# Optimization experiments

Hardware: AMD Instinct MI355X
Metric: run time of the kernel (lower is better)

The kernel has to match this reference:

```python
import jax, jax.numpy as jnp
import numpy as np

R, B, D, H, N, F = 8, 16, 32, 128, 2048, 256
HALF_LOG_2PI = np.float32(0.9189385332046727)  # 0.5*log(2*pi)


def _made_masks():
    # MADE masks for a 2-hidden-layer network (D -> H -> H -> 2*D), params=2,
    # input_order='random' per (region, batch) network, hidden degrees cyclic in [1, D-1].
    rng = np.random.RandomState(0)
    deg_in = np.stack([np.stack([rng.permutation(D) + 1 for _ in range(B)]) for _ in range(R)])  # [R,B,D]
    h_deg = (np.arange(H) % (D - 1)) + 1  # [H]
    M1 = (deg_in[:, :, :, None] <= h_deg[None, None, None, :]).astype(np.float32)  # [R,B,D,H]
    M2 = np.broadcast_to((h_deg[:, None] <= h_deg[None, :]).astype(np.float32), (R, B, H, H)).copy()  # [R,B,H,H]
    out_deg = np.repeat(deg_in, 2, axis=-1)  # [R,B,2D]; index k=2*d+p matches reshape(...,D,2)
    M3 = (h_deg[None, None, :, None] < out_deg[:, :, None, :]).astype(np.float32)  # [R,B,H,2D]
    return M1, M2, M3


def setup_inputs() -> dict:
    key = jax.random.key(0)
    k1, k2, k3, k4 = jax.random.split(key, 4)
    x = jax.random.normal(k1, (N, F), dtype=jnp.float32)
    W1 = jax.random.normal(k2, (R, B, D, H), dtype=jnp.float32) * 0.1
    W2 = jax.random.normal(k3, (R, B, H, H), dtype=jnp.float32) * 0.05
    W3 = jax.random.normal(k4, (R, B, H, 2 * D), dtype=jnp.float32) * 0.02
    M1, M2, M3 = _made_masks()
    region_idx = jnp.arange(F, dtype=jnp.int64 if jax.config.jax_enable_x64 else jnp.int32).reshape(R, D)
    return {"x": x, "W1": W1, "W2": W2, "W3": W3,
            "M1": jnp.asarray(M1), "M2": jnp.asarray(M2), "M3": jnp.asarray(M3),
            "region_idx": region_idx}


def reference(x, W1, W2, W3, M1, M2, M3, region_idx):
    # Gather per-region features: [N, R, D] -> [R, N, D]
    xr = jnp.transpose(x[:, region_idx], (1, 0, 2))
    # Masked MADE forward (no bias, relu), batched over all R*B networks.
    h1 = jax.nn.relu(jnp.einsum('rnd,rbdh->rbnh', xr, W1 * M1))
    h2 = jax.nn.relu(jnp.einsum('rbnh,rbhk->rbnk', h1, W2 * M2))
    out = jnp.einsum('rbnk,rbko->rbno', h2, W3 * M3)  # [R,B,N,2D]
    out = out.reshape(out.shape[0], out.shape[1], out.shape[2], -1, 2)  # [R,B,N,D,2]
    shift, log_scale = out[..., 0], out[..., 1]
    # MAF inverse (one pass): u = (y - shift) * exp(-log_scale);
    # log_prob = sum_d Normal(0,1).log_prob(u_d) - log_scale_d
    u = (xr[:, None] - shift) * jnp.exp(-log_scale)  # [R,B,N,D]
    ll = jnp.sum(-0.5 * u * u - HALF_LOG_2PI - log_scale, axis=-1)  # [R,B,N]
    return jnp.transpose(ll, (2, 0, 1))  # [N, R, B]
```

## Files before the change

### kernel.cpp

```cpp
#include <hip/hip_runtime.h>
#include <math.h>

constexpr int R_ = 8;
constexpr int B_ = 16;
constexpr int D_ = 32;
constexpr int H_ = 128;
constexpr int N_ = 2048;
constexpr int F_ = 256;
constexpr int O_ = 64;
constexpr float HLP_ = 0.9189385332046727f;

typedef float f32x4 __attribute__((ext_vector_type(4)));
typedef short bf16x8 __attribute__((ext_vector_type(8)));
typedef unsigned uint32x4 __attribute__((ext_vector_type(4)));

__device__ __forceinline__ unsigned pk2(float lo, float hi) {
    unsigned a = __builtin_bit_cast(unsigned, lo) + 0x8000u;
    unsigned b = __builtin_bit_cast(unsigned, hi) + 0x8000u;
    return __builtin_amdgcn_perm(b, a, 0x07060302);
}

__global__ __launch_bounds__(256, 1)
void flow_all(const float* __restrict__ x,
              const float* __restrict__ W1, const float* __restrict__ W2,
              const float* __restrict__ W3,
              const float* __restrict__ M1, const float* __restrict__ M2,
              const float* __restrict__ M3,
              const int* __restrict__ ridx,
              float* __restrict__ out)
{
    __shared__ __align__(16) unsigned short stg[2][5120];
    __shared__ __align__(16) unsigned short hws[4][8192];

    const int bid = blockIdx.x;
    const int rb  = bid >> 1;
    const int hf  = bid & 1;
    const int r   = rb >> 4;

    const int t    = threadIdx.x;
    const int lane = t & 63;
    const int w    = t >> 6;
    const int q    = lane >> 4;
    const int c    = lane & 15;

    unsigned short* hwp = hws[w];

    const int nbase = hf * 1024 + w * 256 + c;
    const int xoff = r * 32 + q * 8;

    auto xload = [&](int row, float* g) {
        const float* p0 = x + (size_t)row * F_ + xoff;
        float4 f0 = *(const float4*)p0;
        float4 f1 = *(const float4*)(p0 + 4);
        g[0] = f0.x; g[1] = f0.y; g[2] = f0.z; g[3] = f0.w;
        g[4] = f1.x; g[5] = f1.y; g[6] = f1.z; g[7] = f1.w;
    };

    float g0A[8], g0B[8], g1A[8], g1B[8];
    xload(nbase, g0A);
    xload(nbase + 16, g0B);

    bf16x8 a1[8], a2[4][8], a3[4][4];
    {
        const float* W1b = W1 + (size_t)rb * 32 * 128;
        const float* M1b = M1 + (size_t)rb * 32 * 128;
        const float* W2b = W2 + (size_t)rb * 128 * 128;
        const float* M2s = M2;
        const float* W3b = W3 + (size_t)rb * 128 * 64;
        const float* M3b = M3 + (size_t)rb * 128 * 64;

        const int pm  = t & 127, pkh = t >> 7;
        const int qm  = t & 63,  qk  = t >> 6;
        int osrc;
        {
            int dp = qm >> 1, pb = qm & 1;
            int dsrc = ((dp >> 1) & 3) * 8 + (dp >> 3) * 2 + (dp & 1);
            osrc = dsrc * 2 + pb;
        }

        float wv[2][16], mv[2][16];
        auto slab_load = [&](int s, float* wvv, float* mvv) {
            if (s == 0) {
                const float* wp = W1b + (size_t)(pkh * 16) * 128 + pm;
                const float* mp = M1b + (size_t)(pkh * 16) * 128 + pm;
#pragma unroll
                for (int e = 0; e < 16; ++e) { wvv[e] = wp[(size_t)e * 128]; mvv[e] = mp[(size_t)e * 128]; }
            } else if (s <= 4) {
                const float* wp = W2b + (size_t)((s - 1) * 32 + pkh * 16) * 128 + pm;
                const float* mp = M2s + (size_t)((s - 1) * 32 + pkh * 16) * 128 + pm;
#pragma unroll
                for (int e = 0; e < 16; ++e) { wvv[e] = wp[(size_t)e * 128]; mvv[e] = mp[(size_t)e * 128]; }
            } else {
                int ss = s - 5;
                const float* wp = W3b + (size_t)(ss * 64 + qk * 16) * 64 + osrc;
                const float* mp = M3b + (size_t)(ss * 64 + qk * 16) * 64 + osrc;
#pragma unroll
                for (int e = 0; e < 16; ++e) { wvv[e] = wp[(size_t)e * 64]; mvv[e] = mp[(size_t)e * 64]; }
            }
        };
        auto slab_store = [&](int s, const float* wvv, const float* mvv) {
            unsigned u[8];
#pragma unroll
            for (int e2 = 0; e2 < 8; ++e2)
                u[e2] = pk2(wvv[2 * e2] * mvv[2 * e2], wvv[2 * e2 + 1] * mvv[2 * e2 + 1]);
            uint32x4 ulo = {u[0], u[1], u[2], u[3]};
            uint32x4 uhi = {u[4], u[5], u[6], u[7]};
            unsigned short* st = stg[s & 1];
            if (s <= 4) {
                *(uint32x4*)&st[pm * 40 + pkh * 16]     = ulo;
                *(uint32x4*)&st[pm * 40 + pkh * 16 + 8] = uhi;
            } else {
                *(uint32x4*)&st[qm * 72 + qk * 16]     = ulo;
                *(uint32x4*)&st[qm * 72 + qk * 16 + 8] = uhi;
            }
        };

        slab_load(0, wv[0], mv[0]);
#pragma unroll
        for (int s = 0; s < 7; ++s) {
            if (s < 6) slab_load(s + 1, wv[(s + 1) & 1], mv[(s + 1) & 1]);
            slab_store(s, wv[s & 1], mv[s & 1]);
            __syncthreads();
            const unsigned short* st = stg[s & 1];
            if (s == 0) {
#pragma unroll
                for (int mt = 0; mt < 8; ++mt)
                    a1[mt] = *(const bf16x8*)&st[(mt * 16 + c) * 40 + q * 8];
            } else if (s <= 4) {
#pragma unroll
                for (int mt = 0; mt < 8; ++mt)
                    a2[s - 1][mt] = *(const bf16x8*)&st[(mt * 16 + c) * 40 + q * 8];
            } else {
                int ss = s - 5;
#pragma unroll
                for (int mt3 = 0; mt3 < 4; ++mt3) {
                    a3[ss * 2 + 0][mt3] = *(const bf16x8*)&st[(mt3 * 16 + c) * 72 + 0  + q * 8];
                    a3[ss * 2 + 1][mt3] = *(const bf16x8*)&st[(mt3 * 16 + c) * 72 + 32 + q * 8];
                }
            }
        }
    }

    auto hstore = [&](int tau, int mt, const f32x4& v) {
        int ktw = mt >> 1;
        int qw  = (mt & 1) * 2 + (q >> 1);
        int j0  = (q & 1) * 4;
        unsigned lo = pk2(fmaxf(v[0], 0.f), fmaxf(v[1], 0.f));
        unsigned hi = pk2(fmaxf(v[2], 0.f), fmaxf(v[3], 0.f));
        *(uint2*)&hwp[(((tau * 4 + ktw) * 64) + qw * 16 + c) * 8 + j0] = make_uint2(lo, hi);
    };

    const f32x4 z = {0.f, 0.f, 0.f, 0.f};

    auto pass_body = [&](int p, int tb, const float* xA, const float* xB,
                         float* nA, float* nB) {
        uint32x4 uA = {pk2(xA[0], xA[1]), pk2(xA[2], xA[3]), pk2(xA[4], xA[5]), pk2(xA[6], xA[7])};
        uint32x4 uB = {pk2(xB[0], xB[1]), pk2(xB[2], xB[3]), pk2(xB[4], xB[5]), pk2(xB[6], xB[7])};
        bf16x8 xbA = __builtin_bit_cast(bf16x8, uA);
        bf16x8 xbB = __builtin_bit_cast(bf16x8, uB);

        {
            f32x4 accA[8], accB[8];
#pragma unroll
            for (int mt = 0; mt < 8; ++mt) {
                accA[mt] = __builtin_amdgcn_mfma_f32_16x16x32_bf16(a1[mt], xbA, z, 0, 0, 0);
                accB[mt] = __builtin_amdgcn_mfma_f32_16x16x32_bf16(a1[mt], xbB, z, 0, 0, 0);
            }
#pragma unroll
            for (int mt = 0; mt < 8; ++mt) { hstore(tb + 0, mt, accA[mt]); hstore(tb + 1, mt, accB[mt]); }
        }

        if (p < 7) {
            xload(nbase + (p + 1) * 32, nA);
            xload(nbase + (p + 1) * 32 + 16, nB);
        }

        {
            f32x4 c2A[8], c2B[8];
#pragma unroll
            for (int mt = 0; mt < 8; ++mt) { c2A[mt] = z; c2B[mt] = z; }
#pragma unroll
            for (int kt = 0; kt < 4; ++kt) {
                bf16x8 bA = *(const bf16x8*)&hwp[(((tb + 0) * 4 + kt) * 64 + lane) * 8];
                bf16x8 bB = *(const bf16x8*)&hwp[(((tb + 1) * 4 + kt) * 64 + lane) * 8];
#pragma unroll
                for (int mt = 0; mt < 8; ++mt) {
                    c2A[mt] = __builtin_amdgcn_mfma_f32_16x16x32_bf16(a2[kt][mt], bA, c2A[mt], 0, 0, 0);
                    c2B[mt] = __builtin_amdgcn_mfma_f32_16x16x32_bf16(a2[kt][mt], bB, c2B[mt], 0, 0, 0);
                }
            }
#pragma unroll
            for (int mt = 0; mt < 8; ++mt) { hstore(tb + 0, mt, c2A[mt]); hstore(tb + 1, mt, c2B[mt]); }
        }

        {
            f32x4 c3A[4], c3B[4];
#pragma unroll
            for (int mt3 = 0; mt3 < 4; ++mt3) { c3A[mt3] = z; c3B[mt3] = z; }
#pragma unroll
            for (int kt = 0; kt < 4; ++kt) {
                bf16x8 bA = *(const bf16x8*)&hwp[(((tb + 0) * 4 + kt) * 64 + lane) * 8];
                bf16x8 bB = *(const bf16x8*)&hwp[(((tb + 1) * 4 + kt) * 64 + lane) * 8];
#pragma unroll
                for (int mt3 = 0; mt3 < 4; ++mt3) {
                    c3A[mt3] = __builtin_amdgcn_mfma_f32_16x16x32_bf16(a3[kt][mt3], bA, c3A[mt3], 0, 0, 0);
                    c3B[mt3] = __builtin_amdgcn_mfma_f32_16x16x32_bf16(a3[kt][mt3], bB, c3B[mt3], 0, 0, 0);
                }
            }
            float llA = 0.f, llB = 0.f;
#pragma unroll
            for (int mt3 = 0; mt3 < 4; ++mt3) {
#pragma unroll
                for (int rr = 0; rr < 2; ++rr) {
                    float shA = c3A[mt3][rr * 2], lsA = c3A[mt3][rr * 2 + 1];
                    float shB = c3B[mt3][rr * 2], lsB = c3B[mt3][rr * 2 + 1];
                    float u0 = (xA[mt3 * 2 + rr] - shA) * __expf(-lsA);
                    float u1 = (xB[mt3 * 2 + rr] - shB) * __expf(-lsB);
                    llA += fmaf(-0.5f * u0, u0, -HLP_ - lsA);
                    llB += fmaf(-0.5f * u1, u1, -HLP_ - lsB);
                }
            }
            llA += __shfl_xor(llA, 16, 64);  llA += __shfl_xor(llA, 32, 64);
            llB += __shfl_xor(llB, 16, 64);  llB += __shfl_xor(llB, 32, 64);
            if (q == 0) {
                int n = nbase + p * 32;
                out[(size_t)n * 128 + rb]        = llA;
                out[(size_t)(n + 16) * 128 + rb] = llB;
            }
        }
    };

#pragma unroll 1
    for (int p2 = 0; p2 < 4; ++p2) {
        pass_body(2 * p2,     0, g0A, g0B, g1A, g1B);
        pass_body(2 * p2 + 1, 2, g1A, g1B, g0A, g0B);
    }
}

extern "C" void kernel_launch(void* const* d_in, const int* in_sizes, int n_in,
                              void* d_out, int out_size, void* d_ws, size_t ws_size,
                              hipStream_t stream) {
    const float* x   = (const float*)d_in[0];
    const float* W1  = (const float*)d_in[1];
    const float* W2  = (const float*)d_in[2];
    const float* W3  = (const float*)d_in[3];
    const float* M1  = (const float*)d_in[4];
    const float* M2  = (const float*)d_in[5];
    const float* M3  = (const float*)d_in[6];
    const int*  ridx = (const int*)d_in[7];
    float* out = (float*)d_out;

    flow_all<<<dim3(256), dim3(256), 0, stream>>>(x, W1, W2, W3, M1, M2, M3, ridx, out);
}
```

Before: 111.6 us.

## Split rows across four blocks per network and allow two blocks per CU

Each network (region, batch) is now handled by four blocks of 512 rows instead of two blocks of 1024, so the grid doubles to 512 blocks. The per-wave hidden buffer and register ping-pong are halved, and launch bounds ask for two blocks per CU so more waves can hide latency. The cost is that every block must load and convert the masked weights into registers again, doubling that setup work, and the register cap may cause spills given the large weight fragments held in registers.

```diff
diff --git a/kernel.cpp b/kernel.cpp
--- a/kernel.cpp
+++ b/kernel.cpp
@@ -20,7 +20,7 @@
     return __builtin_amdgcn_perm(b, a, 0x07060302);
 }
 
-__global__ __launch_bounds__(256, 1)
+__global__ __launch_bounds__(256, 2)
 void flow_all(const float* __restrict__ x,
               const float* __restrict__ W1, const float* __restrict__ W2,
               const float* __restrict__ W3,
@@ -30,11 +30,11 @@
               float* __restrict__ out)
 {
     __shared__ __align__(16) unsigned short stg[2][5120];
-    __shared__ __align__(16) unsigned short hws[4][8192];
+    __shared__ __align__(16) unsigned short hws[4][4096];
 
     const int bid = blockIdx.x;
-    const int rb  = bid >> 1;
-    const int hf  = bid & 1;
+    const int rb  = bid >> 2;
+    const int sl  = bid & 3;
     const int r   = rb >> 4;
 
     const int t    = threadIdx.x;
@@ -45,7 +45,7 @@
 
     unsigned short* hwp = hws[w];
 
-    const int nbase = hf * 1024 + w * 256 + c;
+    const int nbase = sl * 512 + w * 128 + c;
     const int xoff = r * 32 + q * 8;
 
     auto xload = [&](int row, float* g) {
@@ -56,9 +56,9 @@
         g[4] = f1.x; g[5] = f1.y; g[6] = f1.z; g[7] = f1.w;
     };
 
-    float g0A[8], g0B[8], g1A[8], g1B[8];
-    xload(nbase, g0A);
-    xload(nbase + 16, g0B);
+    float gA[8], gB[8];
+    xload(nbase, gA);
+    xload(nbase + 16, gB);
 
     bf16x8 a1[8], a2[4][8], a3[4][4];
     {
@@ -152,8 +152,11 @@
 
     const f32x4 z = {0.f, 0.f, 0.f, 0.f};
 
-    auto pass_body = [&](int p, int tb, const float* xA, const float* xB,
-                         float* nA, float* nB) {
+#pragma unroll 1
+    for (int p = 0; p < 4; ++p) {
+        float xA[8], xB[8];
+#pragma unroll
+        for (int j = 0; j < 8; ++j) { xA[j] = gA[j]; xB[j] = gB[j]; }
         uint32x4 uA = {pk2(xA[0], xA[1]), pk2(xA[2], xA[3]), pk2(xA[4], xA[5]), pk2(xA[6], xA[7])};
         uint32x4 uB = {pk2(xB[0], xB[1]), pk2(xB[2], xB[3]), pk2(xB[4], xB[5]), pk2(xB[6], xB[7])};
         bf16x8 xbA = __builtin_bit_cast(bf16x8, uA);
@@ -167,12 +170,12 @@
                 accB[mt] = __builtin_amdgcn_mfma_f32_16x16x32_bf16(a1[mt], xbB, z, 0, 0, 0);
             }
 #pragma unroll
-            for (int mt = 0; mt < 8; ++mt) { hstore(tb + 0, mt, accA[mt]); hstore(tb + 1, mt, accB[mt]); }
-        }
-
-        if (p < 7) {
-            xload(nbase + (p + 1) * 32, nA);
-            xload(nbase + (p + 1) * 32 + 16, nB);
+            for (int mt = 0; mt < 8; ++mt) { hstore(0, mt, accA[mt]); hstore(1, mt, accB[mt]); }
+        }
+
+        if (p < 3) {
+            xload(nbase + (p + 1) * 32, gA);
+            xload(nbase + (p + 1) * 32 + 16, gB);
         }
 
         {
@@ -181,8 +184,8 @@
             for (int mt = 0; mt < 8; ++mt) { c2A[mt] = z; c2B[mt] = z; }
 #pragma unroll
             for (int kt = 0; kt < 4; ++kt) {
-                bf16x8 bA = *(const bf16x8*)&hwp[(((tb + 0) * 4 + kt) * 64 + lane) * 8];
-                bf16x8 bB = *(const bf16x8*)&hwp[(((tb + 1) * 4 + kt) * 64 + lane) * 8];
+                bf16x8 bA = *(const bf16x8*)&hwp[((0 * 4 + kt) * 64 + lane) * 8];
+                bf16x8 bB = *(const bf16x8*)&hwp[((1 * 4 + kt) * 64 + lane) * 8];
 #pragma unroll
                 for (int mt = 0; mt < 8; ++mt) {
                     c2A[mt] = __builtin_amdgcn_mfma_f32_16x16x32_bf16(a2[kt][mt], bA, c2A[mt], 0, 0, 0);
@@ -190,7 +193,7 @@
                 }
             }
 #pragma unroll
-            for (int mt = 0; mt < 8; ++mt) { hstore(tb + 0, mt, c2A[mt]); hstore(tb + 1, mt, c2B[mt]); }
+            for (int mt = 0; mt < 8; ++mt) { hstore(0, mt, c2A[mt]); hstore(1, mt, c2B[mt]); }
         }
 
         {
@@ -199,8 +202,8 @@
             for (int mt3 = 0; mt3 < 4; ++mt3) { c3A[mt3] = z; c3B[mt3] = z; }
 #pragma unroll
             for (int kt = 0; kt < 4; ++kt) {
-                bf16x8 bA = *(const bf16x8*)&hwp[(((tb + 0) * 4 + kt) * 64 + lane) * 8];
-                bf16x8 bB = *(const bf16x8*)&hwp[(((tb + 1) * 4 + kt) * 64 + lane) * 8];
+                bf16x8 bA = *(const bf16x8*)&hwp[((0 * 4 + kt) * 64 + lane) * 8];
+                bf16x8 bB = *(const bf16x8*)&hwp[((1 * 4 + kt) * 64 + lane) * 8];
 #pragma unroll
                 for (int mt3 = 0; mt3 < 4; ++mt3) {
                     c3A[mt3] = __builtin_amdgcn_mfma_f32_16x16x32_bf16(a3[kt][mt3], bA, c3A[mt3], 0, 0, 0);
@@ -228,12 +231,6 @@
                 out[(size_t)(n + 16) * 128 + rb] = llB;
             }
         }
-    };
-
-#pragma unroll 1
-    for (int p2 = 0; p2 < 4; ++p2) {
-        pass_body(2 * p2,     0, g0A, g0B, g1A, g1B);
-        pass_body(2 * p2 + 1, 2, g1A, g1B, g0A, g0B);
     }
 }
 
@@ -250,5 +247,5 @@
     const int*  ridx = (const int*)d_in[7];
     float* out = (float*)d_out;
 
-    flow_all<<<dim3(256), dim3(256), 0, stream>>>(x, W1, W2, W3, M1, M2, M3, ridx, out);
+    flow_all<<<dim3(512), dim3(256), 0, stream>>>(x, W1, W2, W3, M1, M2, M3, ridx, out);
 }
```

After: 144.4 us. 29.3% more time.
